# Kernel tuning notes

Hardware: AMD Instinct MI355X
Metric: run time of the kernel (lower is better)

Reference implementation:

```python
import jax, jax.numpy as jnp
import numpy as np
from jax import lax

B, L, N = 64, 1024, 64
IN_SZ, MEM_SZ, DEC = 128, 1024, 3


def setup_inputs() -> dict:
    key = jax.random.key(0)
    ks = jax.random.split(key, 8)
    x = jax.random.normal(ks[0], (B, L, N), dtype=jnp.float32)
    # sensor net: Linear(N -> IN_SZ) with bias (stored as [in, out])
    W_sense = jax.random.normal(ks[1], (N, IN_SZ), dtype=jnp.float32) / np.sqrt(N)
    b_sense = jax.random.normal(ks[2], (IN_SZ,), dtype=jnp.float32) * 0.01
    # nBRC: ff_im Linear(IN_SZ -> 3*MEM_SZ, bias=False), ff_mm Linear(MEM_SZ -> 2*MEM_SZ, bias=False)
    W_im = jax.random.normal(ks[3], (IN_SZ, 3 * MEM_SZ), dtype=jnp.float32) / np.sqrt(IN_SZ)
    W_mm = jax.random.normal(ks[4], (MEM_SZ, 2 * MEM_SZ), dtype=jnp.float32) / np.sqrt(MEM_SZ)
    # actor net: Linear(MEM_SZ -> DEC) with bias
    W_act = jax.random.normal(ks[5], (MEM_SZ, DEC), dtype=jnp.float32) / np.sqrt(MEM_SZ)
    b_act = jax.random.normal(ks[6], (DEC,), dtype=jnp.float32) * 0.01
    return {"x": x, "W_sense": W_sense, "b_sense": b_sense,
            "W_im": W_im, "W_mm": W_mm, "W_act": W_act, "b_act": b_act}


def reference(x, W_sense, b_sense, W_im, W_mm, W_act, b_act):
    # sense: applied per-token (flattened in torch; equivalent broadcasted matmul)
    inputs = x @ W_sense + b_sense                      # [B, L, IN_SZ]
    # precompute the input projection for all timesteps in one GEMM
    proj = inputs @ W_im                                 # [B, L, 3*MEM_SZ]
    proj_t = jnp.moveaxis(proj, 1, 0)                    # [L, B, 3*MEM_SZ]
    h0 = jnp.zeros((x.shape[0], MEM_SZ), dtype=x.dtype)

    def step(h, p):
        i_a, i_c, i_o = jnp.split(p, 3, axis=-1)         # each [B, MEM_SZ]
        m = h @ W_mm                                      # [B, 2*MEM_SZ]
        m_a, m_c = jnp.split(m, 2, axis=-1)
        a = 1.0 + jnp.tanh(i_a + m_a)
        c = jax.nn.sigmoid(i_c + m_c)
        hn = c * h + (1.0 - c) * jnp.tanh(i_o + a * h)
        return hn, hn

    _, hs = lax.scan(step, h0, proj_t)                    # [L, B, MEM_SZ]
    memory = jnp.moveaxis(hs, 0, 1)                       # [B, L, MEM_SZ]
    logits = memory @ W_act + b_act                       # [B, L, DEC]
    return jax.nn.softmax(logits, axis=-1)
```

## Files before the change

### kernel.cpp

```cpp
#include <hip/hip_runtime.h>
#include <hip/hip_bf16.h>


#define B_TOT 64
#define L_SEQ 1024
#define N_IN 64
#define INSZ 128
#define MEM 1024
#define DEC 3

#define NGROUP 8
#define BG 8
#define NMEM 32
#define RING 16

typedef __hip_bfloat16 bf16;
typedef short bf16x8 __attribute__((ext_vector_type(8)));
typedef float f32x4 __attribute__((ext_vector_type(4)));
typedef int i32x4 __attribute__((ext_vector_type(4)));
typedef unsigned long long ull;

#define OFF_INPUTS 0
#define SZ_INPUTS  (L_SEQ * 64 * INSZ * 2)
#define OFF_WMM    (OFF_INPUTS + SZ_INPUTS)
#define SZ_WMM     (128 * 32 * 64 * 8 * 2)
#define OFF_WIM    (OFF_WMM + SZ_WMM)
#define SZ_WIM     (192 * 4 * 64 * 8 * 2)
#define OFF_HBUF   (OFF_WIM + SZ_WIM)
#define SZ_HBUF    (RING * NGROUP * BG * MEM * 2)
#define OFF_CTR    (OFF_HBUF + SZ_HBUF)
#define SZ_CTR     ((8192 + 256) * 4)

__device__ __forceinline__ float fast_tanh(float x) {
    float e = __expf(2.f * x);
    return 1.f - 2.f / (e + 1.f);
}
__device__ __forceinline__ float fast_sigmoid(float x) {
    return 1.f / (1.f + __expf(-x));
}

__global__ void k_sense(const float* __restrict__ x, const float* __restrict__ Ws,
                        const float* __restrict__ bs, bf16* __restrict__ inputs) {
    int t = blockIdx.x;
    int tid = threadIdx.x;
    __shared__ float xls[64][64];
    __shared__ float wls[64][128];
    for (int idx = tid; idx < 64 * 64; idx += 256) {
        int b = idx >> 6, k = idx & 63;
        xls[b][k] = x[((size_t)b * L_SEQ + t) * N_IN + k];
    }
    for (int idx = tid; idx < 64 * 128; idx += 256) {
        int k = idx >> 7, j = idx & 127;
        wls[k][j] = Ws[k * INSZ + j];
    }
    __syncthreads();
    int j = tid & 127;
    int bh = tid >> 7;
    float bj = bs[j];
    for (int bi = 0; bi < 32; ++bi) {
        int b = bh * 32 + bi;
        float acc = bj;
#pragma unroll
        for (int k = 0; k < 64; ++k) acc += xls[b][k] * wls[k][j];
        inputs[((size_t)t * 64 + b) * INSZ + j] = (bf16)acc;
    }
}

__global__ void k_pack(const float* __restrict__ Wmm, const float* __restrict__ Wim,
                       bf16* __restrict__ pmm, bf16* __restrict__ pim) {
    int idx = blockIdx.x * 256 + threadIdx.x;
    const int NMMF = 128 * 32 * 64 * 8;
    if (idx < NMMF) {
        int j = idx & 7, lane = (idx >> 3) & 63, kb = (idx >> 9) & 31, ct = idx >> 14;
        int n = ct * 16 + (lane & 15);
        int k = kb * 32 + ((lane >> 4) << 3) + j;
        pmm[idx] = (bf16)Wmm[(size_t)k * 2048 + n];
    } else {
        int idx2 = idx - NMMF;
        if (idx2 < 192 * 4 * 64 * 8) {
            int j = idx2 & 7, lane = (idx2 >> 3) & 63, kb = (idx2 >> 9) & 3, ct = idx2 >> 11;
            int n = ct * 16 + (lane & 15);
            int k = kb * 32 + ((lane >> 4) << 3) + j;
            pim[idx2] = (bf16)Wim[(size_t)k * 3072 + n];
        }
    }
}

__launch_bounds__(256, 1)
__global__ void k_main(const bf16* __restrict__ inputs, const bf16* __restrict__ pmm,
                       const bf16* __restrict__ pim, const float* __restrict__ Wact,
                       const float* __restrict__ bact, bf16* __restrict__ hbuf,
                       float* __restrict__ out, unsigned int* __restrict__ ctr) {
    const int g = blockIdx.x & 7;
    const int m = blockIdx.x >> 3;
    const int tid = (int)threadIdx.x;
    const int wave = tid >> 6;
    const int lane = tid & 63;
    const int r16 = lane & 15;
    const int q = lane >> 4;

    __shared__ float ilds[2][3][2][8][16];
    __shared__ float mpart[2][4][4][8][16];
    __shared__ float wact_lds[3072];
    __shared__ float aplds[2][4][3];
    __shared__ float bactl[3];
    __shared__ unsigned idsl[256];
    __shared__ int fflagl;
    __shared__ float outbuf[L_SEQ * 3];

    for (int idx = tid; idx < 3072; idx += 256) wact_lds[idx] = Wact[idx];
    if (tid < 3) bactl[tid] = bact[tid];

    bf16x8 wb[4][8];
    {
        int base_ct[4] = {2 * m, 2 * m + 1, 64 + 2 * m, 65 + 2 * m};
#pragma unroll
        for (int t4 = 0; t4 < 4; ++t4)
#pragma unroll
            for (int kk = 0; kk < 8; ++kk)
                wb[t4][kk] = *(const bf16x8*)(pmm +
                    (((size_t)base_ct[t4] * 32 + (wave * 8 + kk)) * 64 + lane) * 8);
    }
    bf16x8 wi[2][4];
    if (wave < 3) {
#pragma unroll
        for (int tl = 0; tl < 2; ++tl) {
            int ct2 = wave * 64 + m * 2 + tl;
#pragma unroll
            for (int kb2 = 0; kb2 < 4; ++kb2)
                wi[tl][kb2] = *(const bf16x8*)(pim + (((size_t)ct2 * 4 + kb2) * 64 + lane) * 8);
        }
    }

    f32x4 hreg = {0.f, 0.f, 0.f, 0.f};
    const int erow = lane >> 3;
    const int ec = lane & 7;
    const int ep = ec >> 2;
    const int ecl = (ec & 3) * 4;

    unsigned int* flags   = ctr + g * 512;
    unsigned int* flagsL2 = ctr + 4096 + g * 512;
    unsigned int* ids     = ctr + 8192;

    unsigned xid;
    asm volatile("s_getreg_b32 %0, hwreg(HW_REG_XCC_ID)" : "=s"(xid));
    if (tid == 0)
        __hip_atomic_store(&ids[g * 32 + m], xid + 1u, __ATOMIC_RELAXED,
                           __HIP_MEMORY_SCOPE_AGENT);
    if (wave == 0) {
        int sb = 1 << 20;
        unsigned v0 = 0, v1 = 0, v2 = 0, v3 = 0;
        bool all = false;
        while (!all && --sb > 0) {
            v0 = __hip_atomic_load(&ids[lane], __ATOMIC_RELAXED, __HIP_MEMORY_SCOPE_AGENT);
            v1 = __hip_atomic_load(&ids[64 + lane], __ATOMIC_RELAXED, __HIP_MEMORY_SCOPE_AGENT);
            v2 = __hip_atomic_load(&ids[128 + lane], __ATOMIC_RELAXED, __HIP_MEMORY_SCOPE_AGENT);
            v3 = __hip_atomic_load(&ids[192 + lane], __ATOMIC_RELAXED, __HIP_MEMORY_SCOPE_AGENT);
            all = (bool)__all((int)(v0 && v1 && v2 && v3));
        }
        idsl[lane] = v0; idsl[64 + lane] = v1; idsl[128 + lane] = v2; idsl[192 + lane] = v3;
    }
    __syncthreads();
    if (tid == 0) {
        int f = 1;
        for (int g2 = 0; g2 < 8; ++g2) {
            unsigned r = idsl[g2 * 32];
            for (int k2 = 1; k2 < 32; ++k2) f &= (idsl[g2 * 32 + k2] == r);
        }
        fflagl = f;
    }
    __syncthreads();
    const bool fastf = (fflagl != 0);

    bf16x8 afin[4];
    auto load_in = [&](int t) {
        if (wave < 3) {
            int brow = g * 8 + (r16 & 7);
            const bf16* src = inputs + ((size_t)t * 64 + brow) * INSZ + q * 8;
#pragma unroll
            for (int kb2 = 0; kb2 < 4; ++kb2)
                afin[kb2] = *(const bf16x8*)(src + kb2 * 32);
        }
    };
    auto mma_in_deposit = [&](int t) {
        if (wave < 3) {
            f32x4 a0 = (f32x4){0.f, 0.f, 0.f, 0.f};
            f32x4 a1 = (f32x4){0.f, 0.f, 0.f, 0.f};
#pragma unroll
            for (int kb2 = 0; kb2 < 4; ++kb2) {
                a0 = __builtin_amdgcn_mfma_f32_16x16x32_bf16(afin[kb2], wi[0][kb2], a0, 0, 0, 0);
                a1 = __builtin_amdgcn_mfma_f32_16x16x32_bf16(afin[kb2], wi[1][kb2], a1, 0, 0, 0);
            }
            if (q < 2) {
#pragma unroll
                for (int reg = 0; reg < 4; ++reg) {
                    ilds[t & 1][wave][0][q * 4 + reg][r16] = a0[reg];
                    ilds[t & 1][wave][1][q * 4 + reg][r16] = a1[reg];
                }
            }
        }
    };

    auto poll_own = [&](unsigned target) {
        int k = wave * 8 + (lane & 7);
        bool act = lane < 8;
        unsigned vbest = act ? 0u : target;
        bool done = false;
        int rounds = 0;
        int sb = 1 << 20;
        while (!done && --sb > 0) {
            if (fastf && act && vbest < target) {
                const unsigned* a = flagsL2 + k * 16;
                unsigned vl;
                asm volatile("global_load_dword %0, %1, off sc0\n\t"
                             "s_waitcnt vmcnt(0)"
                             : "=&v"(vl) : "v"(a) : "memory");
                if (vl > vbest) vbest = vl;
            }
            if (act && vbest < target && (!fastf || rounds >= 2)) {
                unsigned vm = __hip_atomic_load(&flags[k * 16], __ATOMIC_RELAXED,
                                                __HIP_MEMORY_SCOPE_AGENT);
                if (vm > vbest) vbest = vm;
            }
            done = (bool)__all((int)(vbest >= target));
            ++rounds;
            if (!done && rounds > 8) __builtin_amdgcn_s_sleep(1);
        }
    };

    auto hload = [&](int t_src, int gg) -> ushort4 {
        int c0 = gg * 4;
        const bf16* hp = hbuf +
            ((size_t)(((t_src & (RING - 1)) * NGROUP + g)) * (BG * MEM)) +
            (c0 >> 5) * 256 + m * 32 + (c0 & 31);
        return *(const ushort4*)hp;
    };
    auto emit_accum = [&](ushort4 hv, int gg, float& p0, float& p1, float& p2) {
        int c0 = gg * 4;
        float h0 = __uint_as_float((unsigned)hv.x << 16);
        float h1 = __uint_as_float((unsigned)hv.y << 16);
        float h2 = __uint_as_float((unsigned)hv.z << 16);
        float h3 = __uint_as_float((unsigned)hv.w << 16);
        const f32x4* wp = (const f32x4*)&wact_lds[c0 * 3];
        f32x4 w0 = wp[0], w1 = wp[1], w2 = wp[2];
        p0 += h0 * w0[0] + h1 * w0[3] + h2 * w1[2] + h3 * w2[1];
        p1 += h0 * w0[1] + h1 * w1[0] + h2 * w1[3] + h3 * w2[2];
        p2 += h0 * w0[2] + h1 * w1[1] + h2 * w2[0] + h3 * w2[3];
    };
    auto emit_reduce = [&](int t_src, float p0, float p1, float p2) {
#pragma unroll
        for (int off = 32; off >= 1; off >>= 1) {
            p0 += __shfl_xor(p0, off);
            p1 += __shfl_xor(p1, off);
            p2 += __shfl_xor(p2, off);
        }
        if (lane == 0) {
            aplds[t_src & 1][wave][0] = p0;
            aplds[t_src & 1][wave][1] = p1;
            aplds[t_src & 1][wave][2] = p2;
        }
    };
    auto fin = [&](int tout) {
        int pr = tout & 1;
        float l0 = aplds[pr][0][0] + aplds[pr][1][0] + aplds[pr][2][0] + bactl[0];
        float l1 = aplds[pr][0][1] + aplds[pr][1][1] + aplds[pr][2][1] + bactl[1];
        float l2 = aplds[pr][0][2] + aplds[pr][1][2] + aplds[pr][2][2] + bactl[2];
        float mx = fmaxf(l0, fmaxf(l1, l2));
        float e0 = __expf(l0 - mx), e1 = __expf(l1 - mx), e2 = __expf(l2 - mx);
        float inv = 1.f / (e0 + e1 + e2);
        outbuf[tout * 3 + 0] = e0 * inv;
        outbuf[tout * 3 + 1] = e1 * inv;
        outbuf[tout * 3 + 2] = e2 * inv;
    };

    auto ew_publish = [&](int t) {
        int par = t & 1;
        f32x4 ma = *(const f32x4*)&mpart[par][0][ep][erow][ecl];
        f32x4 mc = *(const f32x4*)&mpart[par][0][2 + ep][erow][ecl];
#pragma unroll
        for (int w = 1; w < 4; ++w) {
            ma += *(const f32x4*)&mpart[par][w][ep][erow][ecl];
            mc += *(const f32x4*)&mpart[par][w][2 + ep][erow][ecl];
        }
        f32x4 ia = *(const f32x4*)&ilds[par][0][ep][erow][ecl];
        f32x4 ic = *(const f32x4*)&ilds[par][1][ep][erow][ecl];
        f32x4 io = *(const f32x4*)&ilds[par][2][ep][erow][ecl];
        bf16 hb[4];
#pragma unroll
        for (int i = 0; i < 4; ++i) {
            float a = 1.f + fast_tanh(ia[i] + ma[i]);
            float c = fast_sigmoid(ic[i] + mc[i]);
            float hn = c * hreg[i] + (1.f - c) * fast_tanh(io[i] + a * hreg[i]);
            hreg[i] = hn;
            hb[i] = (bf16)hn;
        }
        ull v = *(const ull*)hb;
        bf16* base = hbuf +
            ((size_t)(((t & (RING - 1)) * NGROUP + g)) * (BG * MEM)) + m * 256;
        ull* dst = (ull*)base + lane;
        if (fastf) {
            *dst = v;
        } else {
            __hip_atomic_store(dst, v, __ATOMIC_RELAXED, __HIP_MEMORY_SCOPE_AGENT);
        }
        asm volatile("s_waitcnt vmcnt(0)" ::: "memory");
        if (lane == 0) {
            if (fastf) flagsL2[m * 16] = (unsigned)(t + 1);
            __hip_atomic_store(&flags[m * 16], (unsigned)(t + 1), __ATOMIC_RELAXED,
                               __HIP_MEMORY_SCOPE_AGENT);
        }
    };

    load_in(0);
    mma_in_deposit(0);
    load_in(1);

#pragma clang loop unroll(disable)
    for (int t = 0; t < L_SEQ; ++t) {
        if (t != 0 && (t & (RING - 1)) == 0)
            __builtin_amdgcn_fence(__ATOMIC_ACQUIRE, "agent");

        if (t > 0) poll_own((unsigned)t);

        {
            const bf16* lp = hbuf +
                ((size_t)((((t - 1) & (RING - 1)) * NGROUP + g)) * (BG * MEM)) +
                (size_t)(wave * 8) * 256 + ((r16 & 7) * 32 + q * 8);
            bf16x8 af[8];
#pragma unroll
            for (int kk = 0; kk < 8; ++kk)
                af[kk] = *(const bf16x8*)(lp + kk * 256);
            f32x4 acc0 = {0.f, 0.f, 0.f, 0.f};
            f32x4 acc1 = {0.f, 0.f, 0.f, 0.f};
            f32x4 acc2 = {0.f, 0.f, 0.f, 0.f};
            f32x4 acc3 = {0.f, 0.f, 0.f, 0.f};
#pragma unroll
            for (int kk = 0; kk < 8; ++kk) {
                acc0 = __builtin_amdgcn_mfma_f32_16x16x32_bf16(af[kk], wb[0][kk], acc0, 0, 0, 0);
                acc1 = __builtin_amdgcn_mfma_f32_16x16x32_bf16(af[kk], wb[1][kk], acc1, 0, 0, 0);
                acc2 = __builtin_amdgcn_mfma_f32_16x16x32_bf16(af[kk], wb[2][kk], acc2, 0, 0, 0);
                acc3 = __builtin_amdgcn_mfma_f32_16x16x32_bf16(af[kk], wb[3][kk], acc3, 0, 0, 0);
            }
            if (q < 2) {
#pragma unroll
                for (int reg = 0; reg < 4; ++reg) {
                    mpart[t & 1][wave][0][q * 4 + reg][r16] = acc0[reg];
                    mpart[t & 1][wave][1][q * 4 + reg][r16] = acc1[reg];
                    mpart[t & 1][wave][2][q * 4 + reg][r16] = acc2[reg];
                    mpart[t & 1][wave][3][q * 4 + reg][r16] = acc3[reg];
                }
            }
        }
        ushort4 eh0;
        if (m < 8 && t > 0 && wave < 3) eh0 = hload(t - 1, tid);
        __syncthreads();

        if (wave == 3) {
            ew_publish(t);
        } else {
            ushort4 eh1;
            if (m < 8 && t > 0 && wave == 0) eh1 = hload(t - 1, tid + 192);
            if (t + 1 < L_SEQ) mma_in_deposit(t + 1);
            if (t + 2 < L_SEQ) load_in(t + 2);
            if (m < 8) {
                if (t >= 2 && tid == 64) fin(t - 2);
                if (t > 0) {
                    float p0 = 0.f, p1 = 0.f, p2 = 0.f;
                    emit_accum(eh0, tid, p0, p1, p2);
                    if (wave == 0) emit_accum(eh1, tid + 192, p0, p1, p2);
                    emit_reduce(t - 1, p0, p1, p2);
                }
            }
        }
    }

    if (m < 8) {
        __syncthreads();
        if (tid == 64) fin(L_SEQ - 2);
        poll_own((unsigned)L_SEQ);
        __builtin_amdgcn_fence(__ATOMIC_ACQUIRE, "agent");
        __syncthreads();
        if (wave < 3) {
            float p0 = 0.f, p1 = 0.f, p2 = 0.f;
            ushort4 a = hload(L_SEQ - 1, tid);
            emit_accum(a, tid, p0, p1, p2);
            if (wave == 0) {
                ushort4 b = hload(L_SEQ - 1, tid + 192);
                emit_accum(b, tid + 192, p0, p1, p2);
            }
            emit_reduce(L_SEQ - 1, p0, p1, p2);
        }
        __syncthreads();
        if (tid == 0) fin(L_SEQ - 1);
        __syncthreads();
        float* obase = out + (size_t)(g * 8 + m) * L_SEQ * 3;
        for (int idx = tid; idx < L_SEQ * 3; idx += 256)
            obase[idx] = outbuf[idx];
    }
}

extern "C" void kernel_launch(void* const* d_in, const int* in_sizes, int n_in,
                              void* d_out, int out_size, void* d_ws, size_t ws_size,
                              hipStream_t stream) {
    const float* x    = (const float*)d_in[0];
    const float* Ws   = (const float*)d_in[1];
    const float* bs   = (const float*)d_in[2];
    const float* Wim  = (const float*)d_in[3];
    const float* Wmm  = (const float*)d_in[4];
    const float* Wact = (const float*)d_in[5];
    const float* bact = (const float*)d_in[6];

    char* ws = (char*)d_ws;
    bf16* inputs = (bf16*)(ws + OFF_INPUTS);
    bf16* pmm    = (bf16*)(ws + OFF_WMM);
    bf16* pim    = (bf16*)(ws + OFF_WIM);
    bf16* hbuf   = (bf16*)(ws + OFF_HBUF);
    unsigned int* ctr = (unsigned int*)(ws + OFF_CTR);

    hipMemsetAsync(hbuf, 0, SZ_HBUF, stream);
    hipMemsetAsync(ctr, 0, SZ_CTR, stream);

    k_sense<<<L_SEQ, 256, 0, stream>>>(x, Ws, bs, inputs);
    k_pack<<<(128 * 32 * 64 * 8 + 192 * 4 * 64 * 8) / 256, 256, 0, stream>>>(Wmm, Wim, pmm, pim);
    k_main<<<NGROUP * NMEM, 256, 0, stream>>>(inputs, pmm, pim, Wact, bact, hbuf,
                                              (float*)d_out, ctr);
}
```

Before: 3.051 ms.

## Embed step tags in hidden-state slots instead of separate flag polling

Each published 4-element bf16 hidden chunk now carries the timestep number in interleaved 32-bit words, so consumers poll the data itself rather than separate per-block flag arrays. This removes the flag store, the wait for the data store to complete, and the serialized flag-then-data round trip on the critical recurrence path. Per-wave MFMA partials are now summed with LDS atomicAdd into a zeroed accumulator instead of a 4-way reduction in the elementwise wave. The ring shrinks to 8 and the backoff is more aggressive. The trade-off is twice the hbuf traffic, reliance on 16-byte store atomicity, and extra LDS atomics.

```diff
diff --git a/kernel.cpp b/kernel.cpp
--- a/kernel.cpp
+++ b/kernel.cpp
@@ -12,7 +12,7 @@
 #define NGROUP 8
 #define BG 8
 #define NMEM 32
-#define RING 16
+#define RING 8
 
 typedef __hip_bfloat16 bf16;
 typedef short bf16x8 __attribute__((ext_vector_type(8)));
@@ -27,9 +27,9 @@
 #define OFF_WIM    (OFF_WMM + SZ_WMM)
 #define SZ_WIM     (192 * 4 * 64 * 8 * 2)
 #define OFF_HBUF   (OFF_WIM + SZ_WIM)
-#define SZ_HBUF    (RING * NGROUP * BG * MEM * 2)
+#define SZ_HBUF    (RING * NGROUP * NMEM * 1024)
 #define OFF_CTR    (OFF_HBUF + SZ_HBUF)
-#define SZ_CTR     ((8192 + 256) * 4)
+#define SZ_CTR     (256 * 4)
 
 __device__ __forceinline__ float fast_tanh(float x) {
     float e = __expf(2.f * x);
@@ -37,6 +37,11 @@
 }
 __device__ __forceinline__ float fast_sigmoid(float x) {
     return 1.f / (1.f + __expf(-x));
+}
+
+__device__ __forceinline__ void poll_backoff(int rounds) {
+    if (rounds > 64) __builtin_amdgcn_s_sleep(32);
+    else if (rounds > 8) __builtin_amdgcn_s_sleep(2);
 }
 
 __global__ void k_sense(const float* __restrict__ x, const float* __restrict__ Ws,
@@ -98,9 +103,10 @@
     const int lane = tid & 63;
     const int r16 = lane & 15;
     const int q = lane >> 4;
+    const int slotA = (r16 & 7) * 8 + 2 * q;
 
     __shared__ float ilds[2][3][2][8][16];
-    __shared__ float mpart[2][4][4][8][16];
+    __shared__ float macc[2][2][8][32];
     __shared__ float wact_lds[3072];
     __shared__ float aplds[2][4][3];
     __shared__ float bactl[3];
@@ -109,6 +115,7 @@
     __shared__ float outbuf[L_SEQ * 3];
 
     for (int idx = tid; idx < 3072; idx += 256) wact_lds[idx] = Wact[idx];
+    for (int idx = tid; idx < 1024; idx += 256) ((float*)macc)[idx] = 0.f;
     if (tid < 3) bactl[tid] = bact[tid];
 
     bf16x8 wb[4][8];
@@ -138,9 +145,7 @@
     const int ep = ec >> 2;
     const int ecl = (ec & 3) * 4;
 
-    unsigned int* flags   = ctr + g * 512;
-    unsigned int* flagsL2 = ctr + 4096 + g * 512;
-    unsigned int* ids     = ctr + 8192;
+    unsigned int* ids = ctr;
 
     unsigned xid;
     asm volatile("s_getreg_b32 %0, hwreg(HW_REG_XCC_ID)" : "=s"(xid));
@@ -201,46 +206,20 @@
         }
     };
 
-    auto poll_own = [&](unsigned target) {
-        int k = wave * 8 + (lane & 7);
-        bool act = lane < 8;
-        unsigned vbest = act ? 0u : target;
-        bool done = false;
-        int rounds = 0;
-        int sb = 1 << 20;
-        while (!done && --sb > 0) {
-            if (fastf && act && vbest < target) {
-                const unsigned* a = flagsL2 + k * 16;
-                unsigned vl;
-                asm volatile("global_load_dword %0, %1, off sc0\n\t"
-                             "s_waitcnt vmcnt(0)"
-                             : "=&v"(vl) : "v"(a) : "memory");
-                if (vl > vbest) vbest = vl;
-            }
-            if (act && vbest < target && (!fastf || rounds >= 2)) {
-                unsigned vm = __hip_atomic_load(&flags[k * 16], __ATOMIC_RELAXED,
-                                                __HIP_MEMORY_SCOPE_AGENT);
-                if (vm > vbest) vbest = vm;
-            }
-            done = (bool)__all((int)(vbest >= target));
-            ++rounds;
-            if (!done && rounds > 8) __builtin_amdgcn_s_sleep(1);
-        }
-    };
-
-    auto hload = [&](int t_src, int gg) -> ushort4 {
+    auto actor_load = [&](int t_src, int gg) -> ull {
         int c0 = gg * 4;
-        const bf16* hp = hbuf +
-            ((size_t)(((t_src & (RING - 1)) * NGROUP + g)) * (BG * MEM)) +
-            (c0 >> 5) * 256 + m * 32 + (c0 & 31);
-        return *(const ushort4*)hp;
-    };
-    auto emit_accum = [&](ushort4 hv, int gg, float& p0, float& p1, float& p2) {
+        const char* ap = (const char*)hbuf +
+            ((size_t)(((t_src & (RING - 1)) * NGROUP + g)) * (NMEM * 1024)) +
+            (size_t)(c0 >> 5) * 1024 + ((size_t)(m * 8 + ((c0 >> 2) & 7))) * 16;
+        i32x4 l = *(const i32x4*)ap;
+        return (ull)(unsigned)l.x | ((ull)(unsigned)l.z << 32);
+    };
+    auto emit_accum = [&](ull hv, int gg, float& p0, float& p1, float& p2) {
         int c0 = gg * 4;
-        float h0 = __uint_as_float((unsigned)hv.x << 16);
-        float h1 = __uint_as_float((unsigned)hv.y << 16);
-        float h2 = __uint_as_float((unsigned)hv.z << 16);
-        float h3 = __uint_as_float((unsigned)hv.w << 16);
+        float h0 = __uint_as_float(((unsigned)hv & 0xffffu) << 16);
+        float h1 = __uint_as_float((unsigned)hv & 0xffff0000u);
+        float h2 = __uint_as_float(((unsigned)(hv >> 32) & 0xffffu) << 16);
+        float h3 = __uint_as_float((unsigned)(hv >> 48) << 16);
         const f32x4* wp = (const f32x4*)&wact_lds[c0 * 3];
         f32x4 w0 = wp[0], w1 = wp[1], w2 = wp[2];
         p0 += h0 * w0[0] + h1 * w0[3] + h2 * w1[2] + h3 * w2[1];
@@ -273,63 +252,47 @@
         outbuf[tout * 3 + 2] = e2 * inv;
     };
 
-    auto ew_publish = [&](int t) {
-        int par = t & 1;
-        f32x4 ma = *(const f32x4*)&mpart[par][0][ep][erow][ecl];
-        f32x4 mc = *(const f32x4*)&mpart[par][0][2 + ep][erow][ecl];
-#pragma unroll
-        for (int w = 1; w < 4; ++w) {
-            ma += *(const f32x4*)&mpart[par][w][ep][erow][ecl];
-            mc += *(const f32x4*)&mpart[par][w][2 + ep][erow][ecl];
-        }
-        f32x4 ia = *(const f32x4*)&ilds[par][0][ep][erow][ecl];
-        f32x4 ic = *(const f32x4*)&ilds[par][1][ep][erow][ecl];
-        f32x4 io = *(const f32x4*)&ilds[par][2][ep][erow][ecl];
-        bf16 hb[4];
-#pragma unroll
-        for (int i = 0; i < 4; ++i) {
-            float a = 1.f + fast_tanh(ia[i] + ma[i]);
-            float c = fast_sigmoid(ic[i] + mc[i]);
-            float hn = c * hreg[i] + (1.f - c) * fast_tanh(io[i] + a * hreg[i]);
-            hreg[i] = hn;
-            hb[i] = (bf16)hn;
-        }
-        ull v = *(const ull*)hb;
-        bf16* base = hbuf +
-            ((size_t)(((t & (RING - 1)) * NGROUP + g)) * (BG * MEM)) + m * 256;
-        ull* dst = (ull*)base + lane;
-        if (fastf) {
-            *dst = v;
-        } else {
-            __hip_atomic_store(dst, v, __ATOMIC_RELAXED, __HIP_MEMORY_SCOPE_AGENT);
-        }
-        asm volatile("s_waitcnt vmcnt(0)" ::: "memory");
-        if (lane == 0) {
-            if (fastf) flagsL2[m * 16] = (unsigned)(t + 1);
-            __hip_atomic_store(&flags[m * 16], (unsigned)(t + 1), __ATOMIC_RELAXED,
-                               __HIP_MEMORY_SCOPE_AGENT);
-        }
-    };
-
     load_in(0);
     mma_in_deposit(0);
     load_in(1);
 
+    ull eh0 = 0, eh1 = 0;
+
 #pragma clang loop unroll(disable)
     for (int t = 0; t < L_SEQ; ++t) {
-        if (t != 0 && (t & (RING - 1)) == 0)
-            __builtin_amdgcn_fence(__ATOMIC_ACQUIRE, "agent");
-
-        if (t > 0) poll_own((unsigned)t);
-
+        bf16x8 af[8];
         {
-            const bf16* lp = hbuf +
-                ((size_t)((((t - 1) & (RING - 1)) * NGROUP + g)) * (BG * MEM)) +
-                (size_t)(wave * 8) * 256 + ((r16 & 7) * 32 + q * 8);
-            bf16x8 af[8];
-#pragma unroll
-            for (int kk = 0; kk < 8; ++kk)
-                af[kk] = *(const bf16x8*)(lp + kk * 256);
+            const char* sb2 = (const char*)hbuf +
+                ((size_t)(((t + RING - 1) & (RING - 1)) * NGROUP + g)) * (NMEM * 1024);
+            const char* b0 = sb2 + (size_t)(wave * 8192) + (size_t)slotA * 16;
+            i32x4 l[16];
+            const unsigned tg = (unsigned)t;
+            int rounds = 0;
+            int sbnd = 1 << 17;
+            while (--sbnd > 0) {
+                __builtin_amdgcn_fence(__ATOMIC_ACQUIRE, "agent");
+#pragma unroll
+                for (int i = 0; i < 16; ++i) {
+                    const char* a = b0 + (i >> 1) * 1024 + (i & 1) * 16;
+                    l[i] = *(const i32x4*)a;
+                }
+                bool ok = true;
+#pragma unroll
+                for (int i = 0; i < 16; ++i)
+                    ok &= ((unsigned)l[i].y == tg) & ((unsigned)l[i].w == tg);
+                if (__all((int)ok)) break;
+                poll_backoff(++rounds);
+            }
+#pragma unroll
+            for (int kk = 0; kk < 8; ++kk) {
+                i32x4 d;
+                d.x = l[2 * kk].x;     d.y = l[2 * kk].z;
+                d.z = l[2 * kk + 1].x; d.w = l[2 * kk + 1].z;
+                af[kk] = *(bf16x8*)&d;
+            }
+        }
+
+        {
             f32x4 acc0 = {0.f, 0.f, 0.f, 0.f};
             f32x4 acc1 = {0.f, 0.f, 0.f, 0.f};
             f32x4 acc2 = {0.f, 0.f, 0.f, 0.f};
@@ -342,24 +305,65 @@
                 acc3 = __builtin_amdgcn_mfma_f32_16x16x32_bf16(af[kk], wb[3][kk], acc3, 0, 0, 0);
             }
             if (q < 2) {
+                int par = t & 1;
 #pragma unroll
                 for (int reg = 0; reg < 4; ++reg) {
-                    mpart[t & 1][wave][0][q * 4 + reg][r16] = acc0[reg];
-                    mpart[t & 1][wave][1][q * 4 + reg][r16] = acc1[reg];
-                    mpart[t & 1][wave][2][q * 4 + reg][r16] = acc2[reg];
-                    mpart[t & 1][wave][3][q * 4 + reg][r16] = acc3[reg];
+                    atomicAdd(&macc[par][0][q * 4 + reg][r16], acc0[reg]);
+                    atomicAdd(&macc[par][0][q * 4 + reg][16 + r16], acc1[reg]);
+                    atomicAdd(&macc[par][1][q * 4 + reg][r16], acc2[reg]);
+                    atomicAdd(&macc[par][1][q * 4 + reg][16 + r16], acc3[reg]);
                 }
             }
         }
-        ushort4 eh0;
-        if (m < 8 && t > 0 && wave < 3) eh0 = hload(t - 1, tid);
+        if (m < 8 && t > 0 && wave < 3) eh0 = actor_load(t - 1, tid);
         __syncthreads();
 
         if (wave == 3) {
-            ew_publish(t);
+            int par = t & 1;
+            f32x4 ma = *(const f32x4*)&macc[par][0][erow][ec * 4];
+            f32x4 mc = *(const f32x4*)&macc[par][1][erow][ec * 4];
+            f32x4 ia = *(const f32x4*)&ilds[par][0][ep][erow][ecl];
+            f32x4 ic = *(const f32x4*)&ilds[par][1][ep][erow][ecl];
+            f32x4 io = *(const f32x4*)&ilds[par][2][ep][erow][ecl];
+            bf16 hb[4];
+#pragma unroll
+            for (int i = 0; i < 4; ++i) {
+                float a = 1.f + fast_tanh(ia[i] + ma[i]);
+                float c = fast_sigmoid(ic[i] + mc[i]);
+                float hn = c * hreg[i] + (1.f - c) * fast_tanh(io[i] + a * hreg[i]);
+                hreg[i] = hn;
+                hb[i] = (bf16)hn;
+            }
+            ull v = *(const ull*)hb;
+            char* slotp = (char*)hbuf +
+                ((size_t)(((t & (RING - 1)) * NGROUP + g)) * (NMEM * 1024)) +
+                (size_t)m * 1024 + (size_t)lane * 16;
+            unsigned lo = (unsigned)(v & 0xffffffffu);
+            unsigned hi = (unsigned)(v >> 32);
+            if (fastf) {
+                i32x4 pv;
+                pv.x = (int)lo;
+                pv.y = t + 1;
+                pv.z = (int)hi;
+                pv.w = t + 1;
+                *(i32x4*)slotp = pv;
+            } else {
+                __hip_atomic_store((unsigned*)slotp, lo, __ATOMIC_RELAXED,
+                                   __HIP_MEMORY_SCOPE_AGENT);
+                __hip_atomic_store((unsigned*)(slotp + 8), hi, __ATOMIC_RELAXED,
+                                   __HIP_MEMORY_SCOPE_AGENT);
+                asm volatile("s_waitcnt vmcnt(0)" ::: "memory");
+                __hip_atomic_store((unsigned*)(slotp + 4), (unsigned)(t + 1),
+                                   __ATOMIC_RELAXED, __HIP_MEMORY_SCOPE_AGENT);
+                __hip_atomic_store((unsigned*)(slotp + 12), (unsigned)(t + 1),
+                                   __ATOMIC_RELAXED, __HIP_MEMORY_SCOPE_AGENT);
+            }
+            float* mz = (float*)&macc[par][0][0][0];
+            f32x4 z4 = {0.f, 0.f, 0.f, 0.f};
+            *(f32x4*)(mz + lane * 8) = z4;
+            *(f32x4*)(mz + lane * 8 + 4) = z4;
         } else {
-            ushort4 eh1;
-            if (m < 8 && t > 0 && wave == 0) eh1 = hload(t - 1, tid + 192);
+            if (m < 8 && t > 0 && wave == 0) eh1 = actor_load(t - 1, tid + 192);
             if (t + 1 < L_SEQ) mma_in_deposit(t + 1);
             if (t + 2 < L_SEQ) load_in(t + 2);
             if (m < 8) {
@@ -377,15 +381,30 @@
     if (m < 8) {
         __syncthreads();
         if (tid == 64) fin(L_SEQ - 2);
-        poll_own((unsigned)L_SEQ);
-        __builtin_amdgcn_fence(__ATOMIC_ACQUIRE, "agent");
-        __syncthreads();
+        auto ep_load = [&](int gg) -> ull {
+            int c0 = gg * 4;
+            const char* ap = (const char*)hbuf +
+                ((size_t)((((L_SEQ - 1) & (RING - 1)) * NGROUP + g)) * (NMEM * 1024)) +
+                (size_t)(c0 >> 5) * 1024 + ((size_t)(m * 8 + ((c0 >> 2) & 7))) * 16;
+            i32x4 l;
+            l.x = 0; l.y = 0; l.z = 0; l.w = 0;
+            int sbnd = 1 << 17;
+            int rounds = 0;
+            while (--sbnd > 0) {
+                __builtin_amdgcn_fence(__ATOMIC_ACQUIRE, "agent");
+                l = *(const i32x4*)ap;
+                if ((unsigned)l.y == (unsigned)L_SEQ &&
+                    (unsigned)l.w == (unsigned)L_SEQ) break;
+                poll_backoff(++rounds);
+            }
+            return (ull)(unsigned)l.x | ((ull)(unsigned)l.z << 32);
+        };
         if (wave < 3) {
             float p0 = 0.f, p1 = 0.f, p2 = 0.f;
-            ushort4 a = hload(L_SEQ - 1, tid);
+            ull a = ep_load(tid);
             emit_accum(a, tid, p0, p1, p2);
             if (wave == 0) {
-                ushort4 b = hload(L_SEQ - 1, tid + 192);
+                ull b = ep_load(tid + 192);
                 emit_accum(b, tid + 192, p0, p1, p2);
             }
             emit_reduce(L_SEQ - 1, p0, p1, p2);
```

Measured after the change: 11.28 ms. 3.7x slower.

## Reduce recurrent partials via LDS atomics, drop L2 fast-flag path, add poll backoff

Applied to the files above, without the earlier changes.

Each wave's per-step MFMA partial sums now go into a shared accumulator with LDS atomicAdd, replacing four separate partial buffers that wave 3 summed before the elementwise update. Wave 3 zeroes the accumulator after publishing. The duplicated L2 flag store and its sc0 polling path are removed, leaving only agent-scope flag polling. Polling now backs off with longer sleeps as rounds grow. LDS atomics may serialize, and the longer sleeps can add latency to the cross-block handoff on the recurrence's critical path.

```diff
diff --git a/kernel.cpp b/kernel.cpp
--- a/kernel.cpp
+++ b/kernel.cpp
@@ -29,7 +29,7 @@
 #define OFF_HBUF   (OFF_WIM + SZ_WIM)
 #define SZ_HBUF    (RING * NGROUP * BG * MEM * 2)
 #define OFF_CTR    (OFF_HBUF + SZ_HBUF)
-#define SZ_CTR     ((8192 + 256) * 4)
+#define SZ_CTR     ((4096 + 256) * 4)
 
 __device__ __forceinline__ float fast_tanh(float x) {
     float e = __expf(2.f * x);
@@ -37,6 +37,11 @@
 }
 __device__ __forceinline__ float fast_sigmoid(float x) {
     return 1.f / (1.f + __expf(-x));
+}
+
+__device__ __forceinline__ void poll_backoff(int rounds) {
+    if (rounds > 64) __builtin_amdgcn_s_sleep(32);
+    else if (rounds > 8) __builtin_amdgcn_s_sleep(2);
 }
 
 __global__ void k_sense(const float* __restrict__ x, const float* __restrict__ Ws,
@@ -100,7 +105,7 @@
     const int q = lane >> 4;
 
     __shared__ float ilds[2][3][2][8][16];
-    __shared__ float mpart[2][4][4][8][16];
+    __shared__ float macc[2][2][8][32];
     __shared__ float wact_lds[3072];
     __shared__ float aplds[2][4][3];
     __shared__ float bactl[3];
@@ -109,6 +114,7 @@
     __shared__ float outbuf[L_SEQ * 3];
 
     for (int idx = tid; idx < 3072; idx += 256) wact_lds[idx] = Wact[idx];
+    for (int idx = tid; idx < 1024; idx += 256) ((float*)macc)[idx] = 0.f;
     if (tid < 3) bactl[tid] = bact[tid];
 
     bf16x8 wb[4][8];
@@ -138,9 +144,8 @@
     const int ep = ec >> 2;
     const int ecl = (ec & 3) * 4;
 
-    unsigned int* flags   = ctr + g * 512;
-    unsigned int* flagsL2 = ctr + 4096 + g * 512;
-    unsigned int* ids     = ctr + 8192;
+    unsigned int* flags = ctr + g * 512;
+    unsigned int* ids   = ctr + 4096;
 
     unsigned xid;
     asm volatile("s_getreg_b32 %0, hwreg(HW_REG_XCC_ID)" : "=s"(xid));
@@ -205,30 +210,20 @@
         int k = wave * 8 + (lane & 7);
         bool act = lane < 8;
         unsigned vbest = act ? 0u : target;
-        bool done = false;
         int rounds = 0;
-        int sb = 1 << 20;
-        while (!done && --sb > 0) {
-            if (fastf && act && vbest < target) {
-                const unsigned* a = flagsL2 + k * 16;
-                unsigned vl;
-                asm volatile("global_load_dword %0, %1, off sc0\n\t"
-                             "s_waitcnt vmcnt(0)"
-                             : "=&v"(vl) : "v"(a) : "memory");
-                if (vl > vbest) vbest = vl;
-            }
-            if (act && vbest < target && (!fastf || rounds >= 2)) {
+        int sbnd = 1 << 17;
+        while (--sbnd > 0) {
+            if (act && vbest < target) {
                 unsigned vm = __hip_atomic_load(&flags[k * 16], __ATOMIC_RELAXED,
                                                 __HIP_MEMORY_SCOPE_AGENT);
                 if (vm > vbest) vbest = vm;
             }
-            done = (bool)__all((int)(vbest >= target));
-            ++rounds;
-            if (!done && rounds > 8) __builtin_amdgcn_s_sleep(1);
-        }
-    };
-
-    auto hload = [&](int t_src, int gg) -> ushort4 {
+            if (__all((int)(vbest >= target))) break;
+            poll_backoff(++rounds);
+        }
+    };
+
+    auto actor_load = [&](int t_src, int gg) -> ushort4 {
         int c0 = gg * 4;
         const bf16* hp = hbuf +
             ((size_t)(((t_src & (RING - 1)) * NGROUP + g)) * (BG * MEM)) +
@@ -273,47 +268,11 @@
         outbuf[tout * 3 + 2] = e2 * inv;
     };
 
-    auto ew_publish = [&](int t) {
-        int par = t & 1;
-        f32x4 ma = *(const f32x4*)&mpart[par][0][ep][erow][ecl];
-        f32x4 mc = *(const f32x4*)&mpart[par][0][2 + ep][erow][ecl];
-#pragma unroll
-        for (int w = 1; w < 4; ++w) {
-            ma += *(const f32x4*)&mpart[par][w][ep][erow][ecl];
-            mc += *(const f32x4*)&mpart[par][w][2 + ep][erow][ecl];
-        }
-        f32x4 ia = *(const f32x4*)&ilds[par][0][ep][erow][ecl];
-        f32x4 ic = *(const f32x4*)&ilds[par][1][ep][erow][ecl];
-        f32x4 io = *(const f32x4*)&ilds[par][2][ep][erow][ecl];
-        bf16 hb[4];
-#pragma unroll
-        for (int i = 0; i < 4; ++i) {
-            float a = 1.f + fast_tanh(ia[i] + ma[i]);
-            float c = fast_sigmoid(ic[i] + mc[i]);
-            float hn = c * hreg[i] + (1.f - c) * fast_tanh(io[i] + a * hreg[i]);
-            hreg[i] = hn;
-            hb[i] = (bf16)hn;
-        }
-        ull v = *(const ull*)hb;
-        bf16* base = hbuf +
-            ((size_t)(((t & (RING - 1)) * NGROUP + g)) * (BG * MEM)) + m * 256;
-        ull* dst = (ull*)base + lane;
-        if (fastf) {
-            *dst = v;
-        } else {
-            __hip_atomic_store(dst, v, __ATOMIC_RELAXED, __HIP_MEMORY_SCOPE_AGENT);
-        }
-        asm volatile("s_waitcnt vmcnt(0)" ::: "memory");
-        if (lane == 0) {
-            if (fastf) flagsL2[m * 16] = (unsigned)(t + 1);
-            __hip_atomic_store(&flags[m * 16], (unsigned)(t + 1), __ATOMIC_RELAXED,
-                               __HIP_MEMORY_SCOPE_AGENT);
-        }
-    };
-
     load_in(0);
     mma_in_deposit(0);
     load_in(1);
+
+    ushort4 eh0 = {0, 0, 0, 0}, eh1 = {0, 0, 0, 0};
 
 #pragma clang loop unroll(disable)
     for (int t = 0; t < L_SEQ; ++t) {
@@ -322,14 +281,17 @@
 
         if (t > 0) poll_own((unsigned)t);
 
+        bf16x8 af[8];
         {
             const bf16* lp = hbuf +
-                ((size_t)((((t - 1) & (RING - 1)) * NGROUP + g)) * (BG * MEM)) +
+                ((size_t)((((t + RING - 1) & (RING - 1)) * NGROUP + g)) * (BG * MEM)) +
                 (size_t)(wave * 8) * 256 + ((r16 & 7) * 32 + q * 8);
-            bf16x8 af[8];
 #pragma unroll
             for (int kk = 0; kk < 8; ++kk)
                 af[kk] = *(const bf16x8*)(lp + kk * 256);
+        }
+
+        {
             f32x4 acc0 = {0.f, 0.f, 0.f, 0.f};
             f32x4 acc1 = {0.f, 0.f, 0.f, 0.f};
             f32x4 acc2 = {0.f, 0.f, 0.f, 0.f};
@@ -342,24 +304,54 @@
                 acc3 = __builtin_amdgcn_mfma_f32_16x16x32_bf16(af[kk], wb[3][kk], acc3, 0, 0, 0);
             }
             if (q < 2) {
+                int par = t & 1;
 #pragma unroll
                 for (int reg = 0; reg < 4; ++reg) {
-                    mpart[t & 1][wave][0][q * 4 + reg][r16] = acc0[reg];
-                    mpart[t & 1][wave][1][q * 4 + reg][r16] = acc1[reg];
-                    mpart[t & 1][wave][2][q * 4 + reg][r16] = acc2[reg];
-                    mpart[t & 1][wave][3][q * 4 + reg][r16] = acc3[reg];
+                    atomicAdd(&macc[par][0][q * 4 + reg][r16], acc0[reg]);
+                    atomicAdd(&macc[par][0][q * 4 + reg][16 + r16], acc1[reg]);
+                    atomicAdd(&macc[par][1][q * 4 + reg][r16], acc2[reg]);
+                    atomicAdd(&macc[par][1][q * 4 + reg][16 + r16], acc3[reg]);
                 }
             }
         }
-        ushort4 eh0;
-        if (m < 8 && t > 0 && wave < 3) eh0 = hload(t - 1, tid);
+        if (m < 8 && t > 0 && wave < 3) eh0 = actor_load(t - 1, tid);
         __syncthreads();
 
         if (wave == 3) {
-            ew_publish(t);
+            int par = t & 1;
+            f32x4 ma = *(const f32x4*)&macc[par][0][erow][ec * 4];
+            f32x4 mc = *(const f32x4*)&macc[par][1][erow][ec * 4];
+            f32x4 ia = *(const f32x4*)&ilds[par][0][ep][erow][ecl];
+            f32x4 ic = *(const f32x4*)&ilds[par][1][ep][erow][ecl];
+            f32x4 io = *(const f32x4*)&ilds[par][2][ep][erow][ecl];
+            bf16 hb[4];
+#pragma unroll
+            for (int i = 0; i < 4; ++i) {
+                float a = 1.f + fast_tanh(ia[i] + ma[i]);
+                float c = fast_sigmoid(ic[i] + mc[i]);
+                float hn = c * hreg[i] + (1.f - c) * fast_tanh(io[i] + a * hreg[i]);
+                hreg[i] = hn;
+                hb[i] = (bf16)hn;
+            }
+            ull v = *(const ull*)hb;
+            bf16* base = hbuf +
+                ((size_t)(((t & (RING - 1)) * NGROUP + g)) * (BG * MEM)) + m * 256;
+            ull* dst = (ull*)base + lane;
+            if (fastf) {
+                *dst = v;
+            } else {
+                __hip_atomic_store(dst, v, __ATOMIC_RELAXED, __HIP_MEMORY_SCOPE_AGENT);
+            }
+            asm volatile("s_waitcnt vmcnt(0)" ::: "memory");
+            if (lane == 0)
+                __hip_atomic_store(&flags[m * 16], (unsigned)(t + 1), __ATOMIC_RELAXED,
+                                   __HIP_MEMORY_SCOPE_AGENT);
+            float* mz = (float*)&macc[par][0][0][0];
+            f32x4 z4 = {0.f, 0.f, 0.f, 0.f};
+            *(f32x4*)(mz + lane * 8) = z4;
+            *(f32x4*)(mz + lane * 8 + 4) = z4;
         } else {
-            ushort4 eh1;
-            if (m < 8 && t > 0 && wave == 0) eh1 = hload(t - 1, tid + 192);
+            if (m < 8 && t > 0 && wave == 0) eh1 = actor_load(t - 1, tid + 192);
             if (t + 1 < L_SEQ) mma_in_deposit(t + 1);
             if (t + 2 < L_SEQ) load_in(t + 2);
             if (m < 8) {
@@ -382,10 +374,10 @@
         __syncthreads();
         if (wave < 3) {
             float p0 = 0.f, p1 = 0.f, p2 = 0.f;
-            ushort4 a = hload(L_SEQ - 1, tid);
+            ushort4 a = actor_load(L_SEQ - 1, tid);
             emit_accum(a, tid, p0, p1, p2);
             if (wave == 0) {
-                ushort4 b = hload(L_SEQ - 1, tid + 192);
+                ushort4 b = actor_load(L_SEQ - 1, tid + 192);
                 emit_accum(b, tid + 192, p0, p1, p2);
             }
             emit_reduce(L_SEQ - 1, p0, p1, p2);
```

Result: slower. 5.478 ms (+79.5%).
